# Optimization experiments

Hardware: AMD Instinct MI355X
Metric: run time of the kernel (lower is better)

The kernel has to match this reference:

```python
import jax, jax.numpy as jnp
import numpy as np

N_NODES = 100000

def _gcn_layer(h, src, dst, norm, W, b, n_nodes):
    # GCNConv: x @ W, then symmetric-normalized scatter-add over edges (incl. self-loops)
    h = h @ W                                  # [N, F_out]
    msg = h[src] * norm[:, None]               # [E_tot, F_out]
    out = jax.ops.segment_sum(msg, dst, num_segments=n_nodes)
    return out + b


def setup_inputs() -> dict:
    key = jax.random.key(0)
    k1, k2, k3, k4 = jax.random.split(key, 4)
    N, E, F_in, H, C = N_NODES, 3200000, 128, 16, 16
    x = jax.random.normal(k1, (N, F_in), dtype=jnp.float32)
    edge_index = jax.random.randint(k2, (2, E), 0, N, dtype=jnp.int64)
    W1 = jax.random.normal(k3, (F_in, H), dtype=jnp.float32) * (1.0 / np.sqrt(F_in))
    b1 = jnp.zeros((H,), dtype=jnp.float32)
    W2 = jax.random.normal(k4, (H, C), dtype=jnp.float32) * (1.0 / np.sqrt(H))
    b2 = jnp.zeros((C,), dtype=jnp.float32)
    return {"x": x, "edge_index": edge_index, "W1": W1, "b1": b1, "W2": W2, "b2": b2}


def reference(x, edge_index, W1, b1, W2, b2):
    N = x.shape[0]
    loops = jnp.arange(N, dtype=edge_index.dtype)
    src = jnp.concatenate([edge_index[0], loops])  # messages flow src -> dst (PyG convention)
    dst = jnp.concatenate([edge_index[1], loops])
    # symmetric normalization: deg^{-1/2}[src] * deg^{-1/2}[dst], deg counted on dst w/ self-loops
    deg = jnp.zeros((N,), dtype=x.dtype).at[dst].add(1.0)
    dinv = jax.lax.rsqrt(jnp.where(deg > 0, deg, 1.0))
    norm = dinv[src] * dinv[dst]                   # [E_tot]

    h = _gcn_layer(x, src, dst, norm, W1, b1, N)
    h = jax.nn.relu(h)
    # F.dropout(training=self.training): eval mode -> identity (deterministic reference)
    h = _gcn_layer(h, src, dst, norm, W2, b2, N)
    return jax.nn.log_softmax(h, axis=1)
```

## Files before the change

kernel.cpp:

```cpp
#include <hip/hip_runtime.h>
#include <hip/hip_bf16.h>
#include <math.h>


#define F_IN 128
#define H 16
#define NPB 128
#define MAX_NB 800
#define NBLK 256
#define BINT 1024
#define SMAX 4864

typedef __hip_bfloat16 bf16;

__device__ __forceinline__ float bflo(unsigned v) { return __uint_as_float(v << 16); }
__device__ __forceinline__ float bfhi(unsigned v) { return __uint_as_float(v & 0xffff0000u); }

__device__ __forceinline__ int swz(int p) { return (p & 7) * 32 + (p >> 3); }

__global__ void histA_kernel(const int* __restrict__ dst, int* __restrict__ hist_t,
                             int E, int NB) {
    __shared__ int h[MAX_NB];
    int b = swz(blockIdx.x);
    long long e0 = (long long)E * b / NBLK;
    long long e1 = (long long)E * (b + 1) / NBLK;
    for (int i = threadIdx.x; i < NB; i += BINT) h[i] = 0;
    __syncthreads();
    for (long long e = e0 + threadIdx.x; e < e1; e += BINT)
        atomicAdd(&h[dst[e] >> 7], 1);
    __syncthreads();
    for (int i = threadIdx.x; i < NB; i += BINT) hist_t[i * NBLK + b] = h[i];
}

__global__ void colscan_kernel(int* __restrict__ hist_t, int* __restrict__ btot) {
    __shared__ int s[NBLK];
    int j = blockIdx.x;
    int t = threadIdx.x;
    int v = hist_t[j * NBLK + t];
    s[t] = v;
    __syncthreads();
    for (int off = 1; off < NBLK; off <<= 1) {
        int w = (t >= off) ? s[t - off] : 0;
        __syncthreads();
        s[t] += w;
        __syncthreads();
    }
    hist_t[j * NBLK + t] = s[t] - v;
    if (t == NBLK - 1) btot[j] = s[t];
}

__global__ void bucketscan_kernel(const int* __restrict__ btot, int* __restrict__ base, int NB) {
    __shared__ int s[1024];
    int t = threadIdx.x;
    s[t] = (t < NB) ? btot[t] : 0;
    __syncthreads();
    for (int off = 1; off < 1024; off <<= 1) {
        int v = (t >= off) ? s[t - off] : 0;
        __syncthreads();
        s[t] += v;
        __syncthreads();
    }
    if (t < NB) base[t] = s[t] - btot[t];
    if (t == NB - 1) base[NB] = s[t];
}

__global__ void binC_kernel(const int* __restrict__ src, const int* __restrict__ dst,
                            const int* __restrict__ hist_t, const int* __restrict__ base,
                            unsigned* __restrict__ packed, int E, int NB) {
    __shared__ int pos[MAX_NB];
    int b = swz(blockIdx.x);
    long long e0 = (long long)E * b / NBLK;
    long long e1 = (long long)E * (b + 1) / NBLK;
    for (int i = threadIdx.x; i < NB; i += BINT)
        pos[i] = base[i] + hist_t[i * NBLK + b];
    __syncthreads();
    for (long long e = e0 + threadIdx.x; e < e1; e += BINT) {
        int d = dst[e];
        int bk = d >> 7;
        int p = atomicAdd(&pos[bk], 1);
        packed[p] = (unsigned)src[e] | ((unsigned)(d & 127) << 17);
    }
}

__global__ void sortcsr_kernel(const unsigned* __restrict__ packed, const int* __restrict__ base,
                               unsigned* __restrict__ sorted, int* __restrict__ rowptr,
                               float* __restrict__ dinv, int N, int E) {
    __shared__ unsigned ssort[SMAX];
    __shared__ int cnt[NPB], offs[NPB], cur[NPB];
    int b = blockIdx.x;
    int e0 = base[b];
    int len = base[b + 1] - e0;
    if (len > SMAX) len = SMAX;
    int T = blockDim.x;

    for (int i = threadIdx.x; i < NPB; i += T) cnt[i] = 0;
    __syncthreads();
    for (int i = threadIdx.x; i < len; i += T)
        atomicAdd(&cnt[packed[e0 + i] >> 17], 1);
    __syncthreads();
    if (threadIdx.x < NPB) offs[threadIdx.x] = cnt[threadIdx.x];
    __syncthreads();
    for (int off = 1; off < NPB; off <<= 1) {
        int v = 0;
        if (threadIdx.x < NPB && threadIdx.x >= off) v = offs[threadIdx.x - off];
        __syncthreads();
        if (threadIdx.x < NPB) offs[threadIdx.x] += v;
        __syncthreads();
    }
    if (threadIdx.x < NPB) {
        int ex = offs[threadIdx.x] - cnt[threadIdx.x];
        cur[threadIdx.x] = ex;
        int node = b * NPB + threadIdx.x;
        if (node < N) {
            rowptr[node] = e0 + ex;
            dinv[node] = rsqrtf(1.0f + (float)cnt[threadIdx.x]);
        }
    }
    __syncthreads();
    for (int i = threadIdx.x; i < len; i += T) {
        unsigned p = packed[e0 + i];
        int pos = atomicAdd(&cur[p >> 17], 1);
        ssort[pos] = p;
    }
    __syncthreads();
    for (int i = threadIdx.x; i < len; i += T) sorted[e0 + i] = ssort[i];
    if (b == 0 && threadIdx.x == 0) rowptr[N] = E;
}

#define XPAD 132
__global__ void xw1_kernel(const float* __restrict__ x, const float* __restrict__ W1,
                           const float* __restrict__ dinv, bf16* __restrict__ u, int n) {
    __shared__ float sW1[F_IN * H];
    __shared__ float sx[16 * XPAD];
    for (int t = threadIdx.x; t < F_IN * H; t += blockDim.x) sW1[t] = W1[t];

    int basei = blockIdx.x * 16;
    for (int idx = threadIdx.x; idx < 512; idx += 256) {
        int r = idx >> 5;
        int kk = (idx & 31) << 2;
        int row = basei + r;
        float4 v = make_float4(0.f, 0.f, 0.f, 0.f);
        if (row < n) v = *(const float4*)(x + (size_t)row * F_IN + kk);
        *(float4*)(sx + r * XPAD + kk) = v;
    }
    __syncthreads();

    int r = threadIdx.x >> 4;
    int j = threadIdx.x & 15;
    int row = basei + r;
    if (row >= n) return;

    const float* xr = sx + r * XPAD;
    float acc = 0.0f;
#pragma unroll 16
    for (int k = 0; k < F_IN; k++) acc += xr[k] * sW1[k * H + j];
    u[(size_t)row * H + j] = __float2bfloat16(dinv[row] * acc);
}

__global__ void gatherfin1_kernel(const unsigned* __restrict__ sorted, const int* __restrict__ rowptr,
                                  const bf16* __restrict__ u, const float* __restrict__ dinv,
                                  const float* __restrict__ b1, const float* __restrict__ W2,
                                  bf16* __restrict__ u2, int N) {
    __shared__ float tile[64 * 16];
    __shared__ float sW2[256];
    __shared__ float sb1[16];
    sW2[threadIdx.x] = W2[threadIdx.x];
    if (threadIdx.x < 16) sb1[threadIdx.x] = b1[threadIdx.x];

    const unsigned* uv = (const unsigned*)u;
    int lane = threadIdx.x & 63;
    int wave = threadIdx.x >> 6;
    int j2 = lane & 7, g = lane >> 3;
    int nodeBase = blockIdx.x * 64 + wave * 16;

    for (int t = 0; t < 16; t++) {
        int node = nodeBase + t;
        float ax = 0.f, ay = 0.f;
        if (node < N) {
            int r0 = rowptr[node], r1 = rowptr[node + 1];
            int k = r0 + g;
            for (; k + 24 < r1; k += 32) {
                unsigned p0 = sorted[k], p1 = sorted[k + 8];
                unsigned p2 = sorted[k + 16], p3 = sorted[k + 24];
                unsigned v0 = uv[(size_t)(p0 & 0x1FFFF) * 8 + j2];
                unsigned v1 = uv[(size_t)(p1 & 0x1FFFF) * 8 + j2];
                unsigned v2 = uv[(size_t)(p2 & 0x1FFFF) * 8 + j2];
                unsigned v3 = uv[(size_t)(p3 & 0x1FFFF) * 8 + j2];
                ax += bflo(v0) + bflo(v1) + bflo(v2) + bflo(v3);
                ay += bfhi(v0) + bfhi(v1) + bfhi(v2) + bfhi(v3);
            }
            for (; k < r1; k += 8) {
                unsigned va = uv[(size_t)(sorted[k] & 0x1FFFF) * 8 + j2];
                ax += bflo(va);
                ay += bfhi(va);
            }
        }
        ax += __shfl_xor(ax, 8);  ay += __shfl_xor(ay, 8);
        ax += __shfl_xor(ax, 16); ay += __shfl_xor(ay, 16);
        ax += __shfl_xor(ax, 32); ay += __shfl_xor(ay, 32);
        if (g == 0) {
            tile[(wave * 16 + t) * 16 + 2 * j2] = ax;
            tile[(wave * 16 + t) * 16 + 2 * j2 + 1] = ay;
        }
    }
    __syncthreads();

    int jj = threadIdx.x & 15;
    for (int rr = 0; rr < 4; rr++) {
        int rl = (threadIdx.x >> 4) + rr * 16;
        int node = blockIdx.x * 64 + rl;
        float h = 0.f, di = 0.f;
        if (node < N) {
            di = dinv[node];
            h = di * (tile[rl * 16 + jj] + __bfloat162float(u[(size_t)node * H + jj])) + sb1[jj];
            h = fmaxf(h, 0.f);
        }
        float acc2 = 0.f;
#pragma unroll
        for (int kk = 0; kk < 16; kk++) {
            float hk = __shfl(h, kk, 16);
            acc2 += hk * sW2[kk * 16 + jj];
        }
        if (node < N) u2[(size_t)node * H + jj] = __float2bfloat16(di * acc2);
    }
}

__global__ void gatherfin2_kernel(const unsigned* __restrict__ sorted, const int* __restrict__ rowptr,
                                  const bf16* __restrict__ u2, const float* __restrict__ dinv,
                                  const float* __restrict__ b2, float* __restrict__ out, int N) {
    __shared__ float tile[64 * 16];
    __shared__ float sb2[16];
    if (threadIdx.x < 16) sb2[threadIdx.x] = b2[threadIdx.x];

    const unsigned* uv = (const unsigned*)u2;
    int lane = threadIdx.x & 63;
    int wave = threadIdx.x >> 6;
    int j2 = lane & 7, g = lane >> 3;
    int nodeBase = blockIdx.x * 64 + wave * 16;

    for (int t = 0; t < 16; t++) {
        int node = nodeBase + t;
        float ax = 0.f, ay = 0.f;
        if (node < N) {
            int r0 = rowptr[node], r1 = rowptr[node + 1];
            int k = r0 + g;
            for (; k + 24 < r1; k += 32) {
                unsigned p0 = sorted[k], p1 = sorted[k + 8];
                unsigned p2 = sorted[k + 16], p3 = sorted[k + 24];
                unsigned v0 = uv[(size_t)(p0 & 0x1FFFF) * 8 + j2];
                unsigned v1 = uv[(size_t)(p1 & 0x1FFFF) * 8 + j2];
                unsigned v2 = uv[(size_t)(p2 & 0x1FFFF) * 8 + j2];
                unsigned v3 = uv[(size_t)(p3 & 0x1FFFF) * 8 + j2];
                ax += bflo(v0) + bflo(v1) + bflo(v2) + bflo(v3);
                ay += bfhi(v0) + bfhi(v1) + bfhi(v2) + bfhi(v3);
            }
            for (; k < r1; k += 8) {
                unsigned va = uv[(size_t)(sorted[k] & 0x1FFFF) * 8 + j2];
                ax += bflo(va);
                ay += bfhi(va);
            }
        }
        ax += __shfl_xor(ax, 8);  ay += __shfl_xor(ay, 8);
        ax += __shfl_xor(ax, 16); ay += __shfl_xor(ay, 16);
        ax += __shfl_xor(ax, 32); ay += __shfl_xor(ay, 32);
        if (g == 0) {
            tile[(wave * 16 + t) * 16 + 2 * j2] = ax;
            tile[(wave * 16 + t) * 16 + 2 * j2 + 1] = ay;
        }
    }
    __syncthreads();

    int jj = threadIdx.x & 15;
    for (int rr = 0; rr < 4; rr++) {
        int rl = (threadIdx.x >> 4) + rr * 16;
        int node = blockIdx.x * 64 + rl;
        if (node >= N) continue;
        float di = dinv[node];
        float v = di * (tile[rl * 16 + jj] + __bfloat162float(u2[(size_t)node * H + jj])) + sb2[jj];

        float m = v;
#pragma unroll
        for (int off = 8; off >= 1; off >>= 1) m = fmaxf(m, __shfl_xor(m, off, 16));
        float ex = __expf(v - m);
        float s = ex;
#pragma unroll
        for (int off = 8; off >= 1; off >>= 1) s += __shfl_xor(s, off, 16);

        out[(size_t)node * H + jj] = v - m - __logf(s);
    }
}

extern "C" void kernel_launch(void* const* d_in, const int* in_sizes, int n_in,
                              void* d_out, int out_size, void* d_ws, size_t ws_size,
                              hipStream_t stream) {
    const float* x = (const float*)d_in[0];
    const int* edge_index = (const int*)d_in[1];
    const float* W1 = (const float*)d_in[2];
    const float* b1 = (const float*)d_in[3];
    const float* W2 = (const float*)d_in[4];
    const float* b2 = (const float*)d_in[5];
    float* out = (float*)d_out;

    const int N = in_sizes[0] / F_IN;
    const int E = in_sizes[1] / 2;
    const int* src = edge_index;
    const int* dst = edge_index + E;
    const int NB = (N + NPB - 1) / NPB;

    float* dinv = (float*)d_ws;
    bf16* u = (bf16*)(dinv + N);
    bf16* u2 = (bf16*)((unsigned*)u + (size_t)N * H / 2);
    unsigned* packed = (unsigned*)((unsigned*)u2 + (size_t)N * H / 2);
    unsigned* sorted = packed + E;
    int* hist_t = (int*)(sorted + E);
    int* rowptr = hist_t + (size_t)MAX_NB * NBLK;
    int* btot = rowptr + N + 1;
    int* base = btot + NB;

    histA_kernel<<<NBLK, BINT, 0, stream>>>(dst, hist_t, E, NB);
    colscan_kernel<<<NB, NBLK, 0, stream>>>(hist_t, btot);
    bucketscan_kernel<<<1, 1024, 0, stream>>>(btot, base, NB);
    binC_kernel<<<NBLK, BINT, 0, stream>>>(src, dst, hist_t, base, packed, E, NB);
    sortcsr_kernel<<<NB, 512, 0, stream>>>(packed, base, sorted, rowptr, dinv, N, E);

    xw1_kernel<<<(N + 15) / 16, 256, 0, stream>>>(x, W1, dinv, u, N);
    gatherfin1_kernel<<<(N + 63) / 64, 256, 0, stream>>>(sorted, rowptr, u, dinv, b1, W2, u2, N);
    gatherfin2_kernel<<<(N + 63) / 64, 256, 0, stream>>>(sorted, rowptr, u2, dinv, b2, out, N);
}
```

Measured before the change: 251.1 us.

## Software-pipeline CSR gather by prefetching next node's indices and features

Restructures the per-node neighbor gather in both aggregation kernels into a software pipeline. While the current node's prefetched features are accumulated, the row pointers and up to six index entries of the next node are loaded, and its first feature words are issued afterwards. This hides the dependent-load latency of rowptr, then index, then feature. The cost is more registers per thread, which may lower occupancy, and a serial tail loop for nodes with degree above 48.

```diff
diff --git a/kernel.cpp b/kernel.cpp
--- a/kernel.cpp
+++ b/kernel.cpp
@@ -10,6 +10,7 @@
 #define NBLK 256
 #define BINT 1024
 #define SMAX 4864
+#define PFD 6
 
 typedef __hip_bfloat16 bf16;
 
@@ -157,6 +158,66 @@
     u[(size_t)row * H + j] = __float2bfloat16(dinv[row] * acc);
 }
 
+#define GATHER_TILE(UVPTR)                                                      \
+    int lane = threadIdx.x & 63;                                                \
+    int wave = threadIdx.x >> 6;                                                \
+    int j2 = lane & 7, g = lane >> 3;                                           \
+    int nodeBase = blockIdx.x * 64 + wave * 16;                                 \
+    int r0c = 0, r1c = 0;                                                       \
+    unsigned svc[PFD]; unsigned uvc[PFD];                                       \
+    {   int node = nodeBase;                                                    \
+        if (node < N) { r0c = rowptr[node]; r1c = rowptr[node + 1]; }           \
+        _Pragma("unroll")                                                       \
+        for (int m = 0; m < PFD; m++) {                                         \
+            int k = r0c + g + 8 * m;                                            \
+            if (k < r1c) svc[m] = sorted[k];                                    \
+        }                                                                       \
+        _Pragma("unroll")                                                       \
+        for (int m = 0; m < PFD; m++) {                                         \
+            int k = r0c + g + 8 * m;                                            \
+            if (k < r1c) uvc[m] = UVPTR[(size_t)(svc[m] & 0x1FFFF) * 8 + j2];   \
+        }                                                                       \
+    }                                                                           \
+    for (int t = 0; t < 16; t++) {                                              \
+        int r0n = 0, r1n = 0;                                                   \
+        unsigned svn[PFD];                                                      \
+        if (t < 15) {                                                           \
+            int nn = nodeBase + t + 1;                                          \
+            if (nn < N) { r0n = rowptr[nn]; r1n = rowptr[nn + 1]; }             \
+            _Pragma("unroll")                                                   \
+            for (int m = 0; m < PFD; m++) {                                     \
+                int k = r0n + g + 8 * m;                                        \
+                if (k < r1n) svn[m] = sorted[k];                                \
+            }                                                                   \
+        }                                                                       \
+        float ax = 0.f, ay = 0.f;                                               \
+        _Pragma("unroll")                                                       \
+        for (int m = 0; m < PFD; m++) {                                         \
+            int k = r0c + g + 8 * m;                                            \
+            if (k < r1c) { ax += bflo(uvc[m]); ay += bfhi(uvc[m]); }            \
+        }                                                                       \
+        for (int k = r0c + g + 8 * PFD; k < r1c; k += 8) {                      \
+            unsigned va = UVPTR[(size_t)(sorted[k] & 0x1FFFF) * 8 + j2];        \
+            ax += bflo(va); ay += bfhi(va);                                     \
+        }                                                                       \
+        ax += __shfl_xor(ax, 8);  ay += __shfl_xor(ay, 8);                      \
+        ax += __shfl_xor(ax, 16); ay += __shfl_xor(ay, 16);                     \
+        ax += __shfl_xor(ax, 32); ay += __shfl_xor(ay, 32);                     \
+        if (g == 0) {                                                           \
+            tile[(wave * 16 + t) * 16 + 2 * j2] = ax;                           \
+            tile[(wave * 16 + t) * 16 + 2 * j2 + 1] = ay;                       \
+        }                                                                       \
+        if (t < 15) {                                                           \
+            r0c = r0n; r1c = r1n;                                               \
+            _Pragma("unroll")                                                   \
+            for (int m = 0; m < PFD; m++) {                                     \
+                int k = r0n + g + 8 * m;                                        \
+                svc[m] = svn[m];                                                \
+                if (k < r1n) uvc[m] = UVPTR[(size_t)(svn[m] & 0x1FFFF) * 8 + j2]; \
+            }                                                                   \
+        }                                                                       \
+    }
+
 __global__ void gatherfin1_kernel(const unsigned* __restrict__ sorted, const int* __restrict__ rowptr,
                                   const bf16* __restrict__ u, const float* __restrict__ dinv,
                                   const float* __restrict__ b1, const float* __restrict__ W2,
@@ -167,42 +228,8 @@
     sW2[threadIdx.x] = W2[threadIdx.x];
     if (threadIdx.x < 16) sb1[threadIdx.x] = b1[threadIdx.x];
 
-    const unsigned* uv = (const unsigned*)u;
-    int lane = threadIdx.x & 63;
-    int wave = threadIdx.x >> 6;
-    int j2 = lane & 7, g = lane >> 3;
-    int nodeBase = blockIdx.x * 64 + wave * 16;
-
-    for (int t = 0; t < 16; t++) {
-        int node = nodeBase + t;
-        float ax = 0.f, ay = 0.f;
-        if (node < N) {
-            int r0 = rowptr[node], r1 = rowptr[node + 1];
-            int k = r0 + g;
-            for (; k + 24 < r1; k += 32) {
-                unsigned p0 = sorted[k], p1 = sorted[k + 8];
-                unsigned p2 = sorted[k + 16], p3 = sorted[k + 24];
-                unsigned v0 = uv[(size_t)(p0 & 0x1FFFF) * 8 + j2];
-                unsigned v1 = uv[(size_t)(p1 & 0x1FFFF) * 8 + j2];
-                unsigned v2 = uv[(size_t)(p2 & 0x1FFFF) * 8 + j2];
-                unsigned v3 = uv[(size_t)(p3 & 0x1FFFF) * 8 + j2];
-                ax += bflo(v0) + bflo(v1) + bflo(v2) + bflo(v3);
-                ay += bfhi(v0) + bfhi(v1) + bfhi(v2) + bfhi(v3);
-            }
-            for (; k < r1; k += 8) {
-                unsigned va = uv[(size_t)(sorted[k] & 0x1FFFF) * 8 + j2];
-                ax += bflo(va);
-                ay += bfhi(va);
-            }
-        }
-        ax += __shfl_xor(ax, 8);  ay += __shfl_xor(ay, 8);
-        ax += __shfl_xor(ax, 16); ay += __shfl_xor(ay, 16);
-        ax += __shfl_xor(ax, 32); ay += __shfl_xor(ay, 32);
-        if (g == 0) {
-            tile[(wave * 16 + t) * 16 + 2 * j2] = ax;
-            tile[(wave * 16 + t) * 16 + 2 * j2 + 1] = ay;
-        }
-    }
+    const unsigned* uvp = (const unsigned*)u;
+    GATHER_TILE(uvp)
     __syncthreads();
 
     int jj = threadIdx.x & 15;
@@ -232,42 +259,8 @@
     __shared__ float sb2[16];
     if (threadIdx.x < 16) sb2[threadIdx.x] = b2[threadIdx.x];
 
-    const unsigned* uv = (const unsigned*)u2;
-    int lane = threadIdx.x & 63;
-    int wave = threadIdx.x >> 6;
-    int j2 = lane & 7, g = lane >> 3;
-    int nodeBase = blockIdx.x * 64 + wave * 16;
-
-    for (int t = 0; t < 16; t++) {
-        int node = nodeBase + t;
-        float ax = 0.f, ay = 0.f;
-        if (node < N) {
-            int r0 = rowptr[node], r1 = rowptr[node + 1];
-            int k = r0 + g;
-            for (; k + 24 < r1; k += 32) {
-                unsigned p0 = sorted[k], p1 = sorted[k + 8];
-                unsigned p2 = sorted[k + 16], p3 = sorted[k + 24];
-                unsigned v0 = uv[(size_t)(p0 & 0x1FFFF) * 8 + j2];
-                unsigned v1 = uv[(size_t)(p1 & 0x1FFFF) * 8 + j2];
-                unsigned v2 = uv[(size_t)(p2 & 0x1FFFF) * 8 + j2];
-                unsigned v3 = uv[(size_t)(p3 & 0x1FFFF) * 8 + j2];
-                ax += bflo(v0) + bflo(v1) + bflo(v2) + bflo(v3);
-                ay += bfhi(v0) + bfhi(v1) + bfhi(v2) + bfhi(v3);
-            }
-            for (; k < r1; k += 8) {
-                unsigned va = uv[(size_t)(sorted[k] & 0x1FFFF) * 8 + j2];
-                ax += bflo(va);
-                ay += bfhi(va);
-            }
-        }
-        ax += __shfl_xor(ax, 8);  ay += __shfl_xor(ay, 8);
-        ax += __shfl_xor(ax, 16); ay += __shfl_xor(ay, 16);
-        ax += __shfl_xor(ax, 32); ay += __shfl_xor(ay, 32);
-        if (g == 0) {
-            tile[(wave * 16 + t) * 16 + 2 * j2] = ax;
-            tile[(wave * 16 + t) * 16 + 2 * j2 + 1] = ay;
-        }
-    }
+    const unsigned* uvp = (const unsigned*)u2;
+    GATHER_TILE(uvp)
     __syncthreads();
 
     int jj = threadIdx.x & 15;
```

Measured after the change: 241.9 us. 1.04x faster.
